# Kernel tuning notes

Hardware: AMD Instinct MI355X
Metric: run time of the kernel (lower is better)

## Reference

```python
import jax, jax.numpy as jnp
import numpy as np

B, N, D = 8, 4096, 256
MLP_DIM = int(2.0 * D * 2)  # mlp_expansion_factor * dim * 2


def setup_inputs() -> dict:
    key = jax.random.key(0)
    ks = jax.random.split(key, 16)
    s = 0.02  # small init for MLP linears (torch Linear default is small-uniform)
    return {
        'h':  jax.random.normal(ks[0], (B, N, D), jnp.float32),
        'x1': jax.random.normal(ks[1], (B, N, D, 3), jnp.float32),  # degree 1, m=3
        'x2': jax.random.normal(ks[2], (B, N, D, 5), jnp.float32),  # degree 2, m=5
        # per-degree projections (torch.randn init, unscaled, per source)
        'proj1': jax.random.normal(ks[3], (D, D), jnp.float32),
        'proj2': jax.random.normal(ks[4], (D, D), jnp.float32),
        'pre1':  jax.random.normal(ks[5], (D, D), jnp.float32),
        'pre2':  jax.random.normal(ks[6], (D, D), jnp.float32),
        # per-degree 2-layer MLPs: Linear(2D, MLP_DIM) -> SiLU -> Linear(MLP_DIM, 2D)
        'w1_0': jax.random.normal(ks[7], (2 * D, MLP_DIM), jnp.float32) * s,
        'b1_0': jnp.zeros((MLP_DIM,), jnp.float32),
        'w2_0': jax.random.normal(ks[8], (MLP_DIM, 2 * D), jnp.float32) * s,
        'b2_0': jnp.zeros((2 * D,), jnp.float32),
        'w1_1': jax.random.normal(ks[9], (2 * D, MLP_DIM), jnp.float32) * s,
        'b1_1': jnp.zeros((MLP_DIM,), jnp.float32),
        'w2_1': jax.random.normal(ks[10], (MLP_DIM, 2 * D), jnp.float32) * s,
        'b2_1': jnp.zeros((2 * D,), jnp.float32),
    }


def _one_degree(h, x, pre, proj, w1, b1, w2, b2):
    # x: (b, n, d, m); project channels for the invariant branch
    pm = jnp.einsum('bndm,de->bnem', x, pre)            # (b, n, d, m)
    inv = jnp.sqrt(jnp.sum(pm * pm, axis=-1))           # L2 norm over m -> (b, n, d)
    mlp_in = jnp.concatenate([h, inv], axis=-1)         # (b, n, 2d)
    hid = jax.nn.silu(mlp_in @ w1 + b1)                 # (b, n, mlp_dim)
    out = hid @ w2 + b2                                 # (b, n, 2d)
    m1, m2 = out[..., :D], out[..., D:]                 # each (b, n, d)
    p = jnp.einsum('bndm,de->bnem', x, proj)            # (b, n, d, m)
    mod = p * m2[..., None]                             # per-channel gating over m
    return m1, mod


def reference(h, x1, x2, proj1, proj2, pre1, pre2,
              w1_0, b1_0, w2_0, b2_0, w1_1, b1_1, w2_1, b2_1):
    m1_a, mod1 = _one_degree(h, x1, pre1, proj1, w1_0, b1_0, w2_0, b2_0)
    m1_b, mod2 = _one_degree(h, x2, pre2, proj2, w1_1, b1_1, w2_1, b2_1)
    h_new = h + m1_a + m1_b
    return (h_new, x1 + mod1, x2 + mod2)
```

## Files before the change

### kernel.cpp

```cpp
#include <hip/hip_runtime.h>
#include <hip/hip_bf16.h>

#define BN    32768
#define DD    256
#define MLPD  1024
#define TWOD  512

typedef __attribute__((ext_vector_type(8))) short short8;
typedef __attribute__((ext_vector_type(4))) float f32x4;

using bf16 = __hip_bfloat16;

__device__ __forceinline__ float bf2f(bf16 v){ return __bfloat162float(v); }
__device__ __forceinline__ bf16  f2bf(float v){ return __float2bfloat16(v); }

__device__ __forceinline__ void gl_lds16(const bf16* g, bf16* l) {
    __builtin_amdgcn_global_load_lds(
        (const __attribute__((address_space(1))) void*)(g),
        (__attribute__((address_space(3))) void*)(l),
        16, 0, 0);
}

__global__ __launch_bounds__(256) void kprep(
    const float* __restrict__ pre1, const float* __restrict__ pre2,
    const float* __restrict__ proj1, const float* __restrict__ proj2,
    const float* __restrict__ w10, const float* __restrict__ w11,
    const float* __restrict__ w20, const float* __restrict__ w21,
    const float* __restrict__ h,
    bf16* __restrict__ preT, bf16* __restrict__ projT,
    bf16* __restrict__ w1T, bf16* __restrict__ w2T,
    bf16* __restrict__ hbf)
{
    __shared__ float ft[64][68];
    const int tid = threadIdx.x;
    const int bid = blockIdx.x;
    const int row = tid >> 2;
    const int c4  = (tid & 3) * 16;

    auto do_tile = [&](const float* src, int srcld, int r0, int c0,
                       bf16* dst, int dstld) {
        const float* sp = src + (size_t)(r0 + row)*srcld + c0 + c4;
#pragma unroll
        for (int i = 0; i < 4; i++)
            *(float4*)&ft[row][c4 + i*4] = *(const float4*)(sp + i*4);
        __syncthreads();
        bf16* dp = dst + (size_t)(c0 + row)*dstld + r0 + c4;
        short8 v0, v1;
#pragma unroll
        for (int i = 0; i < 8; i++) {
            bf16 b = f2bf(ft[c4 + i][row]);     v0[i] = *(short*)&b;
            bf16 b2 = f2bf(ft[c4 + 8 + i][row]); v1[i] = *(short*)&b2;
        }
        *(short8*)dp = v0;
        *(short8*)(dp + 8) = v1;
    };

    if (bid < 256) {
        int d = bid >> 7, r = bid & 127;
        int kt = r >> 4, jt = r & 15;
        do_tile(d ? w11 : w10, 1024, kt*64, jt*64,
                w1T + (size_t)d*524288, 512);
    } else if (bid < 512) {
        int r = bid - 256;
        int d = r >> 7; r &= 127;
        int kt = r >> 3, nt = r & 7;
        do_tile(d ? w21 : w20, 512, kt*64, nt*64,
                w2T + (size_t)d*524288, 1024);
    } else if (bid < 576) {
        int r = bid - 512;
        int m = r >> 4; r &= 15;
        int kt = r >> 2, et = r & 3;
        const float* src = (m == 0) ? pre1 : (m == 1) ? pre2
                         : (m == 2) ? proj1 : proj2;
        do_tile(src, 256, kt*64, et*64, preT + (size_t)m*65536, 256);
    } else {
        const long base = (long)(bid - 576) * 16384;
#pragma unroll
        for (int it = 0; it < 16; it++) {
            long o = base + it*1024 + tid*4;
            float4 v = *(const float4*)(h + o);
            short vv[4];
#pragma unroll
            for (int j = 0; j < 4; j++) {
                bf16 b = f2bf(((const float*)&v)[j]);
                vv[j] = *(short*)&b;
            }
            *(long*)(hbf + o) = *(long*)vv;
        }
    }
}

template<int M, int ST>
__global__ __launch_bounds__(256) void kxT(const float* __restrict__ x,
                                           char* __restrict__ outb)
{
    __shared__ float raw[8*256*M];
    const int tid = threadIdx.x;
    const long tok0 = (long)blockIdx.x * 8;
    const float4* src = (const float4*)(x + tok0*256*M);
    const int n4 = (8*256*M)/4;
    for (int i = tid; i < n4; i += 256)
        ((float4*)raw)[i] = src[i];
    __syncthreads();
    const int nOut = 8*M*32;
    for (int i = tid; i < nOut; i += 256) {
        int d8 = i & 31;
        int tm = i >> 5;
        int t = tm / M, m = tm - t*M;
        short8 v;
#pragma unroll
        for (int j = 0; j < 8; j++) {
            bf16 bv = f2bf(raw[(t*256 + d8*8 + j)*M + m]);
            v[j] = *reinterpret_cast<short*>(&bv);
        }
        *(short8*)(outb + (size_t)(tok0 + t)*ST + m*512 + d8*16) = v;
    }
}

template<int M, int ST, bool MOD>
__global__ __launch_bounds__(512) void kxg(const char* __restrict__ xtb,
                                           const bf16* __restrict__ Bmat,
                                           bf16* __restrict__ invp,
                                           const bf16* __restrict__ m2p,
                                           float* __restrict__ xout)
{
    __shared__ bf16 As[2*M*512];
    __shared__ bf16 Bs[8192];
    const int tid = threadIdx.x;
    const int lane = tid & 63, w = tid >> 6;
    const int wg = w >> 2, we = w & 3;
    const int lh = lane >> 4, l15 = lane & 15;
    const long tok0 = (long)blockIdx.x * 32;

    f32x4 acc[M][4];
#pragma unroll
    for (int m = 0; m < M; m++)
#pragma unroll
        for (int c = 0; c < 4; c++) acc[m][c] = (f32x4){0.f,0.f,0.f,0.f};

    for (int kc = 0; kc < 8; kc++) {
        for (int m = we; m < M; m += 4) {
            const char* src = xtb + (size_t)(tok0 + wg*16 + (lane >> 2))*ST
                              + m*512 + kc*64 + (lane & 3)*16;
            gl_lds16((const bf16*)src, As + (wg*M + m)*512);
        }
#pragma unroll
        for (int j = 0; j < 2; j++) {
            int row = (w*2 + j)*16 + (lane >> 2);
            gl_lds16(Bmat + row*256 + kc*32 + (lane & 3)*8,
                     Bs + (w*2 + j)*512);
        }
        __syncthreads();
        short8 a[M], b[4];
#pragma unroll
        for (int m = 0; m < M; m++)
            a[m] = *(const short8*)&As[(wg*M + m)*512 + l15*32 + lh*8];
#pragma unroll
        for (int ct = 0; ct < 4; ct++)
            b[ct] = *(const short8*)&Bs[(we*64 + ct*16 + l15)*32 + lh*8];
#pragma unroll
        for (int m = 0; m < M; m++)
#pragma unroll
            for (int ct = 0; ct < 4; ct++)
                acc[m][ct] = __builtin_amdgcn_mfma_f32_16x16x32_bf16(a[m], b[ct], acc[m][ct], 0, 0, 0);
        __syncthreads();
    }

    if constexpr (!MOD) {
#pragma unroll
        for (int ct = 0; ct < 4; ct++) {
#pragma unroll
            for (int i = 0; i < 4; i++) {
                long t = tok0 + wg*16 + lh*4 + i;
                int e = we*64 + ct*16 + l15;
                float s = 0.f;
#pragma unroll
                for (int m = 0; m < M; m++) { float p = acc[m][ct][i]; s += p*p; }
                invp[t*256 + e] = f2bf(sqrtf(s));
            }
        }
    } else {
#pragma unroll
        for (int ct = 0; ct < 4; ct++) {
#pragma unroll
            for (int i = 0; i < 4; i++) {
                long t = tok0 + wg*16 + lh*4 + i;
                int e = we*64 + ct*16 + l15;
                float m2v = bf2f(m2p[t*256 + e]);
                const char* slot = xtb + (size_t)t*ST + e*2;
#pragma unroll
                for (int m = 0; m < M; m++) {
                    float xv = bf2f(*(const bf16*)(slot + m*512));
                    acc[m][ct][i] = xv + acc[m][ct][i]*m2v;
                }
            }
        }
        __syncthreads();
#pragma unroll
        for (int ct = 0; ct < 4; ct++) {
#pragma unroll
            for (int i = 0; i < 4; i++) {
                long t = tok0 + wg*16 + lh*4 + i;
                int e = we*64 + ct*16 + l15;
#pragma unroll
                for (int m = 0; m < M; m++) {
                    long gi = (t*256 + e)*(long)M + m;
                    xout[gi] = acc[m][ct][i];
                }
            }
        }
    }
}

__global__ __launch_bounds__(512) void kmlp1(const bf16* __restrict__ hbf,
                                             const bf16* __restrict__ invws,
                                             const bf16* __restrict__ w1T,
                                             const float* __restrict__ b1_0,
                                             const float* __restrict__ b1_1,
                                             char* __restrict__ x1b,
                                             char* __restrict__ x2b,
                                             bf16* __restrict__ hid1b)
{
    __shared__ bf16 As[128*32];
    __shared__ bf16 Bs[256*32];
    const int tid = threadIdx.x;
    const int lane = tid & 63, w = tid >> 6;
    const int wr = w >> 2, wc = w & 3;
    const int lh = lane >> 4, l15 = lane & 15;

    const int bid   = ((blockIdx.x & 7) << 8) | (blockIdx.x >> 3);
    const int d     = bid >> 10;
    const int r     = bid & 1023;
    const int mtile = r >> 2;
    const int ntile = r & 3;
    const long tok0 = (long)mtile * 128;
    const int  j0   = ntile * 256;

    const bf16* Ahb = hbf   + (size_t)tok0 * 256;
    const bf16* Ain = invws + (size_t)d * BN * 256 + (size_t)tok0 * 256;
    const bf16* Bw  = w1T   + (size_t)d * MLPD * TWOD;
    const float* b1 = d ? b1_1 : b1_0;

    const int srow = tid >> 2;
    const int scol = (tid & 3) * 8;

    f32x4 acc[4][4];
#pragma unroll
    for (int ai = 0; ai < 4; ai++)
#pragma unroll
        for (int bj = 0; bj < 4; bj++) acc[ai][bj] = (f32x4){0.f,0.f,0.f,0.f};

    for (int kc = 0; kc < 16; kc++) {
        {
            const bf16* src = (kc < 8)
                ? Ahb + (size_t)srow*256 + kc*32 + scol
                : Ain + (size_t)srow*256 + (kc - 8)*32 + scol;
            gl_lds16(src, As + w*512);
        }
#pragma unroll
        for (int i = 0; i < 2; i++) {
            gl_lds16(Bw + (size_t)(j0 + i*128 + srow)*512 + kc*32 + scol,
                     Bs + i*4096 + w*512);
        }
        __syncthreads();
        short8 a[4], b[4];
#pragma unroll
        for (int ai = 0; ai < 4; ai++)
            a[ai] = *(const short8*)&As[(wr*64 + ai*16 + l15)*32 + lh*8];
#pragma unroll
        for (int bj = 0; bj < 4; bj++)
            b[bj] = *(const short8*)&Bs[(wc*64 + bj*16 + l15)*32 + lh*8];
#pragma unroll
        for (int ai = 0; ai < 4; ai++)
#pragma unroll
            for (int bj = 0; bj < 4; bj++)
                acc[ai][bj] = __builtin_amdgcn_mfma_f32_16x16x32_bf16(a[ai], b[bj], acc[ai][bj], 0, 0, 0);
        __syncthreads();
    }

#pragma unroll
    for (int ai = 0; ai < 4; ai++) {
#pragma unroll
        for (int bj = 0; bj < 4; bj++) {
#pragma unroll
            for (int i = 0; i < 4; i++) {
                long t = tok0 + wr*64 + ai*16 + lh*4 + i;
                int  j = j0 + wc*64 + bj*16 + l15;
                float v = acc[ai][bj][i] + b1[j];
                float s = v / (1.0f + __expf(-v));
                bf16 sb = f2bf(s);
                if (d == 0) {
                    *(bf16*)(x2b + (size_t)t*5120 + 2560 + j*2) = sb;
                } else {
                    if (j < 768) *(bf16*)(x1b + (size_t)t*3072 + 1536 + j*2) = sb;
                    else         hid1b[t*256 + (j - 768)] = sb;
                }
            }
        }
    }
}

__global__ __launch_bounds__(512) void kmlp2(const char* __restrict__ x1b,
                                             const char* __restrict__ x2b,
                                             const bf16* __restrict__ hid1b,
                                             const bf16* __restrict__ w2T,
                                             const float* __restrict__ b2_0,
                                             const float* __restrict__ b2_1,
                                             const bf16* __restrict__ hbf,
                                             bf16* __restrict__ m2ws,
                                             float* __restrict__ hout)
{
    __shared__ bf16 As[128*32];
    __shared__ bf16 Bs[256*32];
    const int tid = threadIdx.x;
    const int lane = tid & 63, w = tid >> 6;
    const int wr = w >> 2, wc = w & 3;
    const int lh = lane >> 4, l15 = lane & 15;

    const int nb = blockIdx.x;
    int mtile, n0, dm2, nIter;
    bool is_m1;
    if (nb < 256) {
        int b2 = (nb & 7)*32 + (nb >> 3);
        is_m1 = true;  mtile = b2; n0 = 0; dm2 = 0; nIter = 64;
    } else {
        int r = nb - 256;
        int b2 = (r & 7)*64 + (r >> 3);
        is_m1 = false; mtile = b2 >> 1; n0 = 256; dm2 = b2 & 1; nIter = 32;
    }
    const long tok0 = (long)mtile * 128;

    const int srow = tid >> 2;
    const int scol = (tid & 3) * 8;

    f32x4 acc[4][4];
#pragma unroll
    for (int ai = 0; ai < 4; ai++)
#pragma unroll
        for (int bj = 0; bj < 4; bj++) acc[ai][bj] = (f32x4){0.f,0.f,0.f,0.f};

    for (int it = 0; it < nIter; it++) {
        const int d  = is_m1 ? (it >> 5) : dm2;
        const int kk = it & 31;
        {
            const bf16* src;
            if (d == 0)
                src = (const bf16*)(x2b + (size_t)(tok0 + srow)*5120 + 2560
                                    + kk*64 + (tid & 3)*16);
            else if (kk < 24)
                src = (const bf16*)(x1b + (size_t)(tok0 + srow)*3072 + 1536
                                    + kk*64 + (tid & 3)*16);
            else
                src = hid1b + (size_t)(tok0 + srow)*256 + (kk - 24)*32 + scol;
            gl_lds16(src, As + w*512);
        }
        const bf16* Bw = w2T + (size_t)d * TWOD * MLPD;
#pragma unroll
        for (int i = 0; i < 2; i++) {
            gl_lds16(Bw + (size_t)(n0 + i*128 + srow)*MLPD + kk*32 + scol,
                     Bs + i*4096 + w*512);
        }
        __syncthreads();
        short8 a[4], b[4];
#pragma unroll
        for (int ai = 0; ai < 4; ai++)
            a[ai] = *(const short8*)&As[(wr*64 + ai*16 + l15)*32 + lh*8];
#pragma unroll
        for (int bj = 0; bj < 4; bj++)
            b[bj] = *(const short8*)&Bs[(wc*64 + bj*16 + l15)*32 + lh*8];
#pragma unroll
        for (int ai = 0; ai < 4; ai++)
#pragma unroll
            for (int bj = 0; bj < 4; bj++)
                acc[ai][bj] = __builtin_amdgcn_mfma_f32_16x16x32_bf16(a[ai], b[bj], acc[ai][bj], 0, 0, 0);
        __syncthreads();
    }

#pragma unroll
    for (int ai = 0; ai < 4; ai++) {
#pragma unroll
        for (int bj = 0; bj < 4; bj++) {
#pragma unroll
            for (int i = 0; i < 4; i++) {
                long t = tok0 + wr*64 + ai*16 + lh*4 + i;
                int  n = n0 + wc*64 + bj*16 + l15;
                float v = acc[ai][bj][i];
                if (is_m1) {
                    v += b2_0[n] + b2_1[n];
                    hout[t*256 + n] = bf2f(hbf[t*256 + n]) + v;
                } else {
                    v += (dm2 ? b2_1 : b2_0)[n];
                    m2ws[(size_t)dm2 * BN * 256 + t*256 + (n - 256)] = f2bf(v);
                }
            }
        }
    }
}

extern "C" void kernel_launch(void* const* d_in, const int* in_sizes, int n_in,
                              void* d_out, int out_size, void* d_ws, size_t ws_size,
                              hipStream_t stream)
{
    const float* h     = (const float*)d_in[0];
    const float* x1    = (const float*)d_in[1];
    const float* x2    = (const float*)d_in[2];
    const float* proj1 = (const float*)d_in[3];
    const float* proj2 = (const float*)d_in[4];
    const float* pre1  = (const float*)d_in[5];
    const float* pre2  = (const float*)d_in[6];
    const float* w10   = (const float*)d_in[7];
    const float* b10   = (const float*)d_in[8];
    const float* w20   = (const float*)d_in[9];
    const float* b20   = (const float*)d_in[10];
    const float* w11   = (const float*)d_in[11];
    const float* b11   = (const float*)d_in[12];
    const float* w21   = (const float*)d_in[13];
    const float* b21   = (const float*)d_in[14];

    bf16* preT  = (bf16*)d_ws;
    bf16* projT = preT  + 131072;
    bf16* w1T   = projT + 131072;
    bf16* w2T   = w1T   + 1048576;
    bf16* hbf   = w2T   + 1048576;
    bf16* invm2 = hbf   + 8388608;
    bf16* hid1b = invm2 + 16777216;
    if (ws_size < (size_t)35913728 * 2) return;

    float* hout  = (float*)d_out;
    float* x1out = hout + (size_t)8388608;
    float* x2out = hout + (size_t)33554432;
    char* x1b = (char*)x1out;
    char* x2b = (char*)x2out;

    kprep<<<1088, 256, 0, stream>>>(pre1, pre2, proj1, proj2, w10, w11, w20, w21,
                                    h, preT, projT, w1T, w2T, hbf);
    kxT<3, 3072><<<4096, 256, 0, stream>>>(x1, x1b);
    kxT<5, 5120><<<4096, 256, 0, stream>>>(x2, x2b);
    kxg<3, 3072, false><<<1024, 512, 0, stream>>>(x1b, preT, invm2,
                                                  nullptr, nullptr);
    kxg<5, 5120, false><<<1024, 512, 0, stream>>>(x2b, preT + 65536,
                                                  invm2 + (size_t)BN*256,
                                                  nullptr, nullptr);
    kmlp1<<<2048, 512, 0, stream>>>(hbf, invm2, w1T, b10, b11, x1b, x2b, hid1b);
    kmlp2<<<768, 512, 0, stream>>>(x1b, x2b, hid1b, w2T, b20, b21, hbf, invm2, hout);
    kxg<3, 3072, true><<<1024, 512, 0, stream>>>(x1b, projT, nullptr,
                                                 invm2, x1out);
    kxg<5, 5120, true><<<1024, 512, 0, stream>>>(x2b, projT + 65536, nullptr,
                                                 invm2 + (size_t)BN*256, x2out);
}
```

Baseline: 553.3 us.

## Software-pipeline MLP GEMM loads with multi-buffered LDS and explicit vmcnt waits

Both MLP GEMM kernels now prefetch the next B tile and the A tile two steps ahead into double- and triple-buffered LDS. Explicit s_waitcnt vmcnt counts replace the full __syncthreads drain, so global-to-LDS loads overlap the MFMA compute. This costs more LDS per block, 56 KB instead of 24 KB, which may lower occupancy. Correctness also depends on the hand-counted outstanding-load numbers matching the instructions the compiler emits.

```diff
diff --git a/kernel.cpp b/kernel.cpp
--- a/kernel.cpp
+++ b/kernel.cpp
@@ -221,8 +221,8 @@
                                              char* __restrict__ x2b,
                                              bf16* __restrict__ hid1b)
 {
-    __shared__ bf16 As[128*32];
-    __shared__ bf16 Bs[256*32];
+    __shared__ bf16 As[3][4096];
+    __shared__ bf16 Bs[2][8192];
     const int tid = threadIdx.x;
     const int lane = tid & 63, w = tid >> 6;
     const int wr = w >> 2, wc = w & 3;
@@ -250,32 +250,46 @@
 #pragma unroll
         for (int bj = 0; bj < 4; bj++) acc[ai][bj] = (f32x4){0.f,0.f,0.f,0.f};
 
-    for (int kc = 0; kc < 16; kc++) {
-        {
-            const bf16* src = (kc < 8)
-                ? Ahb + (size_t)srow*256 + kc*32 + scol
-                : Ain + (size_t)srow*256 + (kc - 8)*32 + scol;
-            gl_lds16(src, As + w*512);
-        }
-#pragma unroll
-        for (int i = 0; i < 2; i++) {
+    auto stageA = [&](int kc, int buf) {
+        const bf16* src = (kc < 8)
+            ? Ahb + (size_t)srow*256 + kc*32 + scol
+            : Ain + (size_t)srow*256 + (kc - 8)*32 + scol;
+        gl_lds16(src, &As[buf][w*512]);
+    };
+    auto stageB = [&](int kc, int buf) {
+#pragma unroll
+        for (int i = 0; i < 2; i++)
             gl_lds16(Bw + (size_t)(j0 + i*128 + srow)*512 + kc*32 + scol,
-                     Bs + i*4096 + w*512);
-        }
-        __syncthreads();
+                     &Bs[buf][i*4096 + w*512]);
+    };
+    auto compute = [&](int ab, int bb) {
         short8 a[4], b[4];
 #pragma unroll
         for (int ai = 0; ai < 4; ai++)
-            a[ai] = *(const short8*)&As[(wr*64 + ai*16 + l15)*32 + lh*8];
+            a[ai] = *(const short8*)&As[ab][(wr*64 + ai*16 + l15)*32 + lh*8];
 #pragma unroll
         for (int bj = 0; bj < 4; bj++)
-            b[bj] = *(const short8*)&Bs[(wc*64 + bj*16 + l15)*32 + lh*8];
+            b[bj] = *(const short8*)&Bs[bb][(wc*64 + bj*16 + l15)*32 + lh*8];
 #pragma unroll
         for (int ai = 0; ai < 4; ai++)
 #pragma unroll
             for (int bj = 0; bj < 4; bj++)
                 acc[ai][bj] = __builtin_amdgcn_mfma_f32_16x16x32_bf16(a[ai], b[bj], acc[ai][bj], 0, 0, 0);
-        __syncthreads();
+    };
+
+    stageB(0, 0);
+    stageA(0, 0);
+    stageA(1, 1);
+    for (int it = 0; it < 16; it++) {
+        if (it + 1 < 16) stageB(it + 1, (it + 1) & 1);
+        if (it + 2 < 16) stageA(it + 2, (it + 2) % 3);
+        if (it + 2 < 16)      asm volatile("s_waitcnt vmcnt(4)" ::: "memory");
+        else if (it + 1 < 16) asm volatile("s_waitcnt vmcnt(3)" ::: "memory");
+        else                  asm volatile("s_waitcnt vmcnt(0)" ::: "memory");
+        __builtin_amdgcn_s_barrier();
+        compute(it % 3, it & 1);
+        asm volatile("" ::: "memory");
+        __builtin_amdgcn_s_barrier();
     }
 
 #pragma unroll
@@ -310,8 +324,8 @@
                                              bf16* __restrict__ m2ws,
                                              float* __restrict__ hout)
 {
-    __shared__ bf16 As[128*32];
-    __shared__ bf16 Bs[256*32];
+    __shared__ bf16 As[3][4096];
+    __shared__ bf16 Bs[2][8192];
     const int tid = threadIdx.x;
     const int lane = tid & 63, w = tid >> 6;
     const int wr = w >> 2, wc = w & 3;
@@ -339,41 +353,57 @@
 #pragma unroll
         for (int bj = 0; bj < 4; bj++) acc[ai][bj] = (f32x4){0.f,0.f,0.f,0.f};
 
-    for (int it = 0; it < nIter; it++) {
+    auto stageA = [&](int it, int buf) {
         const int d  = is_m1 ? (it >> 5) : dm2;
         const int kk = it & 31;
-        {
-            const bf16* src;
-            if (d == 0)
-                src = (const bf16*)(x2b + (size_t)(tok0 + srow)*5120 + 2560
-                                    + kk*64 + (tid & 3)*16);
-            else if (kk < 24)
-                src = (const bf16*)(x1b + (size_t)(tok0 + srow)*3072 + 1536
-                                    + kk*64 + (tid & 3)*16);
-            else
-                src = hid1b + (size_t)(tok0 + srow)*256 + (kk - 24)*32 + scol;
-            gl_lds16(src, As + w*512);
-        }
+        const bf16* src;
+        if (d == 0)
+            src = (const bf16*)(x2b + (size_t)(tok0 + srow)*5120 + 2560
+                                + kk*64 + (tid & 3)*16);
+        else if (kk < 24)
+            src = (const bf16*)(x1b + (size_t)(tok0 + srow)*3072 + 1536
+                                + kk*64 + (tid & 3)*16);
+        else
+            src = hid1b + (size_t)(tok0 + srow)*256 + (kk - 24)*32 + scol;
+        gl_lds16(src, &As[buf][w*512]);
+    };
+    auto stageB = [&](int it, int buf) {
+        const int d  = is_m1 ? (it >> 5) : dm2;
+        const int kk = it & 31;
         const bf16* Bw = w2T + (size_t)d * TWOD * MLPD;
 #pragma unroll
-        for (int i = 0; i < 2; i++) {
+        for (int i = 0; i < 2; i++)
             gl_lds16(Bw + (size_t)(n0 + i*128 + srow)*MLPD + kk*32 + scol,
-                     Bs + i*4096 + w*512);
-        }
-        __syncthreads();
+                     &Bs[buf][i*4096 + w*512]);
+    };
+    auto compute = [&](int ab, int bb) {
         short8 a[4], b[4];
 #pragma unroll
         for (int ai = 0; ai < 4; ai++)
-            a[ai] = *(const short8*)&As[(wr*64 + ai*16 + l15)*32 + lh*8];
+            a[ai] = *(const short8*)&As[ab][(wr*64 + ai*16 + l15)*32 + lh*8];
 #pragma unroll
         for (int bj = 0; bj < 4; bj++)
-            b[bj] = *(const short8*)&Bs[(wc*64 + bj*16 + l15)*32 + lh*8];
+            b[bj] = *(const short8*)&Bs[bb][(wc*64 + bj*16 + l15)*32 + lh*8];
 #pragma unroll
         for (int ai = 0; ai < 4; ai++)
 #pragma unroll
             for (int bj = 0; bj < 4; bj++)
                 acc[ai][bj] = __builtin_amdgcn_mfma_f32_16x16x32_bf16(a[ai], b[bj], acc[ai][bj], 0, 0, 0);
-        __syncthreads();
+    };
+
+    stageB(0, 0);
+    stageA(0, 0);
+    stageA(1, 1);
+    for (int it = 0; it < nIter; it++) {
+        if (it + 1 < nIter) stageB(it + 1, (it + 1) & 1);
+        if (it + 2 < nIter) stageA(it + 2, (it + 2) % 3);
+        if (it + 2 < nIter)      asm volatile("s_waitcnt vmcnt(4)" ::: "memory");
+        else if (it + 1 < nIter) asm volatile("s_waitcnt vmcnt(3)" ::: "memory");
+        else                     asm volatile("s_waitcnt vmcnt(0)" ::: "memory");
+        __builtin_amdgcn_s_barrier();
+        compute(it % 3, it & 1);
+        asm volatile("" ::: "memory");
+        __builtin_amdgcn_s_barrier();
     }
 
 #pragma unroll
```

After: 581.9 us. 5.2% more time.
